# Kernel tuning notes

Hardware: AMD Instinct MI355X
Metric: run time of the kernel (lower is better)

The kernel has to match this reference:

```python
import jax, jax.numpy as jnp
import numpy as np

N_NODES = 10000
N_EDGES = 320000
D_FEAT = 128          # per-node feature dim -> in_dim = 2*D_FEAT = 256
OUT_DIM = 128
SCALES = 3


def setup_inputs() -> dict:
    key = jax.random.key(0)
    ks = jax.random.split(key, 7)
    node_features = jax.random.normal(ks[0], (N_NODES, D_FEAT), dtype=jnp.float32)
    temporal_info = jax.random.normal(ks[1], (N_NODES,), dtype=jnp.float32)
    in_dim_p1 = 2 * D_FEAT + 1  # 257: concat(src, dest) + temporal gap
    W1 = jax.random.normal(ks[2], (SCALES, in_dim_p1, OUT_DIM), dtype=jnp.float32) * 0.05
    b1 = jax.random.normal(ks[3], (SCALES, OUT_DIM), dtype=jnp.float32) * 0.05
    W2 = jax.random.normal(ks[4], (SCALES, OUT_DIM, OUT_DIM), dtype=jnp.float32) * 0.05
    b2 = jax.random.normal(ks[5], (SCALES, OUT_DIM), dtype=jnp.float32) * 0.05
    edge_index = jax.random.randint(ks[6], (2, N_EDGES), 0, N_NODES, dtype=jnp.int64)
    return {
        "node_features": node_features,
        "temporal_info": temporal_info,
        "W1": W1, "b1": b1, "W2": W2, "b2": b2,
        "edge_index": edge_index,
    }


def reference(node_features, temporal_info, W1, b1, W2, b2, edge_index):
    src, dest = edge_index[0], edge_index[1]
    # gather node pairs + temporal gap -> [E, 2*D+1]
    gap = (temporal_info[src] - temporal_info[dest])[:, None]
    edge_features = jnp.concatenate(
        [node_features[src], node_features[dest], gap], axis=-1)
    # all scales' 2-layer MLPs in one batched einsum; s = scale axis
    h = jax.nn.relu(jnp.einsum('ef,sfo->seo', edge_features, W1) + b1[:, None, :])
    tokens = jnp.einsum('seo,sop->sep', h, W2) + b2[:, None, :]  # [S, E, OUT]
    return tokens.mean(axis=0)  # mean over scales -> [E, OUT]
```

## Files before the change

### kernel.cpp

```cpp
#include <hip/hip_runtime.h>
#include <stdint.h>

#define NN 10000
#define NE 320000
#define DF 128
#define OD 128
#define NS 3

typedef __attribute__((ext_vector_type(8))) short bf16x8;
typedef __attribute__((ext_vector_type(16))) float f32x16;

static __device__ __forceinline__ uint32_t f2bf(float f) {
  uint32_t u = __float_as_uint(f);
  return (u + 0x7FFFu + ((u >> 16) & 1u)) >> 16;
}
static __device__ __forceinline__ float bflo(uint32_t u) { return __uint_as_float(u << 16); }
static __device__ __forceinline__ float bfhi(uint32_t u) { return __uint_as_float(u & 0xFFFF0000u); }

static __device__ __forceinline__ uint32_t relu2(uint32_t a, uint32_t d) {
  float f0 = fmaxf(bflo(a) + bflo(d), 0.0f);
  float f1 = fmaxf(bfhi(a) + bfhi(d), 0.0f);
  return f2bf(f0) | (f2bf(f1) << 16);
}

__global__ __launch_bounds__(256) void prep_w2(
    const float* __restrict__ W2, const float* __restrict__ b2,
    unsigned short* __restrict__ w2t, float* __restrict__ bmean)
{
  int tid = blockIdx.x * 256 + threadIdx.x;
  if (tid < NS * OD * OD) {
    int s = tid / (OD * OD);
    int r = tid % (OD * OD);
    int k = r / OD;
    int n = r % OD;
    w2t[(s * OD + n) * OD + k] = (unsigned short)f2bf(W2[tid]);
  }
  if (tid < OD) bmean[tid] = (b2[tid] + b2[OD + tid] + b2[2 * OD + tid]) * (1.0f / 3.0f);
}

__global__ __launch_bounds__(256) void node_proj(
    const float* __restrict__ nf, const float* __restrict__ temporal,
    const float* __restrict__ W1, const float* __restrict__ b1,
    unsigned short* __restrict__ Qsrc, unsigned short* __restrict__ Qdst)
{
  __shared__ unsigned short Asm[8 * 64 * 8];
  __shared__ unsigned short Bsm[4 * 8 * 64 * 8];
  __shared__ float tsh[32];

  const int t = threadIdx.x;
  const int m0 = blockIdx.x * 32;
  const int c = blockIdx.y;
  const int s = c >> 1, proj = c & 1;

  if (t < 32) {
    int node = m0 + t;
    tsh[t] = (node < NN) ? temporal[node] : 0.0f;
  }

  {
    int m = t >> 3, j16 = t & 7;
    int node = m0 + m;
    float v[16];
    if (node < NN) {
      const float4* p = (const float4*)(nf + (size_t)node * DF + j16 * 16);
      #pragma unroll
      for (int i = 0; i < 4; i++) {
        float4 x = p[i];
        v[4 * i] = x.x; v[4 * i + 1] = x.y; v[4 * i + 2] = x.z; v[4 * i + 3] = x.w;
      }
    } else {
      #pragma unroll
      for (int i = 0; i < 16; i++) v[i] = 0.0f;
    }
    uint32_t pk[8];
    #pragma unroll
    for (int i = 0; i < 8; i++) pk[i] = f2bf(v[2 * i]) | (f2bf(v[2 * i + 1]) << 16);
    uint32_t* d0 = (uint32_t*)(Asm + (j16 * 64 + m) * 8);
    uint32_t* d1 = (uint32_t*)(Asm + (j16 * 64 + 32 + m) * 8);
    d0[0] = pk[0]; d0[1] = pk[1]; d0[2] = pk[2]; d0[3] = pk[3];
    d1[0] = pk[4]; d1[1] = pk[5]; d1[2] = pk[6]; d1[3] = pk[7];
  }

  {
    int o = t & 127, qh = t >> 7;
    const float* wbase = W1 + (size_t)(s * 257 + proj * 128) * OD + o;
    int nt = o >> 5, lnlo = o & 31;
    #pragma unroll
    for (int r = 0; r < 8; r++) {
      int kh = qh * 8 + r;
      float v[8];
      #pragma unroll
      for (int j = 0; j < 8; j++) v[j] = wbase[(size_t)(kh * 8 + j) * OD];
      uint32_t pk[4];
      #pragma unroll
      for (int i = 0; i < 4; i++) pk[i] = f2bf(v[2 * i]) | (f2bf(v[2 * i + 1]) << 16);
      int q = kh >> 1, half = kh & 1;
      uint32_t* d = (uint32_t*)(Bsm + ((nt * 8 + q) * 64 + half * 32 + lnlo) * 8);
      d[0] = pk[0]; d[1] = pk[1]; d[2] = pk[2]; d[3] = pk[3];
    }
  }
  __syncthreads();

  const int lane = t & 63, w = t >> 6;
  f32x16 C;
  #pragma unroll
  for (int i = 0; i < 16; i++) C[i] = 0.0f;
  #pragma unroll
  for (int q = 0; q < 8; q++) {
    bf16x8 a = *(const bf16x8*)(Asm + (q * 64 + lane) * 8);
    bf16x8 b = *(const bf16x8*)(Bsm + ((w * 8 + q) * 64 + lane) * 8);
    C = __builtin_amdgcn_mfma_f32_32x32x16_bf16(a, b, C, 0, 0, 0);
  }

  const int o = w * 32 + (lane & 31);
  const float w1gv = W1[(size_t)(s * 257 + 256) * OD + o];
  const float b1v = b1[s * OD + o];
  unsigned short* Qt = (proj == 0) ? Qsrc : Qdst;
  #pragma unroll
  for (int r = 0; r < 16; r++) {
    int row = (r & 3) + 8 * (r >> 2) + 4 * (lane >> 5);
    int node = m0 + row;
    if (node < NN) {
      float val = C[r];
      if (proj == 0) val += b1v + tsh[row] * w1gv;
      else           val -= tsh[row] * w1gv;
      Qt[(size_t)node * (NS * OD) + s * OD + o] = (unsigned short)f2bf(val);
    }
  }
}

__global__ __launch_bounds__(256) void edge_mlp(
    const unsigned short* __restrict__ Qsrc, const unsigned short* __restrict__ Qdst,
    const unsigned short* __restrict__ W2T, const float* __restrict__ bmean,
    const int* __restrict__ ei, float* __restrict__ out)
{
  __shared__ unsigned short hsm[NS * 8 * 64 * 8];

  const int t = threadIdx.x;
  const int lane = t & 63, w = t >> 6;
  const int nlo = lane & 31, khi = lane >> 5;

  bf16x8 bfrag[NS][8];
  {
    int n = w * 32 + nlo;
    #pragma unroll
    for (int s = 0; s < NS; s++) {
      const unsigned short* base = W2T + ((s * OD + n) * OD + khi * 8);
      #pragma unroll
      for (int q = 0; q < 8; q++)
        bfrag[s][q] = *(const bf16x8*)(base + q * 16);
    }
  }
  const float bmv = bmean[w * 32 + nlo];

  const int m = t >> 3, j16 = t & 7;

  for (int tt = 0; tt < 4; tt++) {
    const int e0 = blockIdx.x * 128 + tt * 32;
    {
      const int e = e0 + m;
      const int srcn = ei[e];
      const int dstn = ei[NE + e];
      const unsigned short* ps = Qsrc + (size_t)srcn * (NS * OD) + j16 * 16;
      const unsigned short* pd = Qdst + (size_t)dstn * (NS * OD) + j16 * 16;
      #pragma unroll
      for (int s = 0; s < NS; s++) {
        uint4 a0 = *(const uint4*)(ps + s * OD);
        uint4 a1 = *(const uint4*)(ps + s * OD + 8);
        uint4 d0 = *(const uint4*)(pd + s * OD);
        uint4 d1 = *(const uint4*)(pd + s * OD + 8);
        uint4 w0, w1;
        w0.x = relu2(a0.x, d0.x); w0.y = relu2(a0.y, d0.y);
        w0.z = relu2(a0.z, d0.z); w0.w = relu2(a0.w, d0.w);
        w1.x = relu2(a1.x, d1.x); w1.y = relu2(a1.y, d1.y);
        w1.z = relu2(a1.z, d1.z); w1.w = relu2(a1.w, d1.w);
        *(uint4*)(hsm + ((s * 8 + j16) * 64 + m) * 8) = w0;
        *(uint4*)(hsm + ((s * 8 + j16) * 64 + 32 + m) * 8) = w1;
      }
    }
    __syncthreads();

    f32x16 C;
    #pragma unroll
    for (int i = 0; i < 16; i++) C[i] = 0.0f;
    #pragma unroll
    for (int s = 0; s < NS; s++) {
      #pragma unroll
      for (int q = 0; q < 8; q++) {
        bf16x8 a = *(const bf16x8*)(hsm + ((s * 8 + q) * 64 + lane) * 8);
        C = __builtin_amdgcn_mfma_f32_32x32x16_bf16(a, bfrag[s][q], C, 0, 0, 0);
      }
    }

    #pragma unroll
    for (int r = 0; r < 16; r++) {
      int row = (r & 3) + 8 * (r >> 2) + 4 * khi;
      out[(size_t)(e0 + row) * OD + w * 32 + nlo] = C[r] * (1.0f / 3.0f) + bmv;
    }
    __syncthreads();
  }
}

extern "C" void kernel_launch(void* const* d_in, const int* in_sizes, int n_in,
                              void* d_out, int out_size, void* d_ws, size_t ws_size,
                              hipStream_t stream) {
  const float* nf       = (const float*)d_in[0];
  const float* temporal = (const float*)d_in[1];
  const float* W1       = (const float*)d_in[2];
  const float* b1       = (const float*)d_in[3];
  const float* W2       = (const float*)d_in[4];
  const float* b2       = (const float*)d_in[5];
  const int*   ei       = (const int*)d_in[6];
  float* out = (float*)d_out;

  char* ws = (char*)d_ws;
  unsigned short* Qsrc = (unsigned short*)ws;
  unsigned short* Qdst = (unsigned short*)(ws + 7680000);
  unsigned short* W2T  = (unsigned short*)(ws + 15360000);
  float*          bmv  = (float*)(ws + 15360000 + 98304);

  prep_w2 <<<dim3(192),     dim3(256), 0, stream>>>(W2, b2, W2T, bmv);
  node_proj<<<dim3(313, 6), dim3(256), 0, stream>>>(nf, temporal, W1, b1, Qsrc, Qdst);
  edge_mlp <<<dim3(2500),   dim3(256), 0, stream>>>(Qsrc, Qdst, W2T, bmv, ei, out);
}
```

Before: 302.5 us.

## Prefetch edge gathers across tiles, swizzle LDS, amortize W1 staging in node_proj

In edge_mlp, all edge indices are loaded up front and the Q gathers for the next 32-edge tile are issued into registers before the MFMA phase of the current tile, so global gather latency overlaps with compute. LDS layouts for the hidden tile and the node-feature tile are XOR-swizzled by k-chunk to reduce bank conflicts. node_proj now loops over 8 node tiles per block with the converted W1 slice held in LDS, amortizing the W1 load and bf16 conversion. The cost is higher register pressure from the double-buffered gather registers, which may reduce occupancy, and fewer node_proj blocks.

```diff
diff --git a/kernel.cpp b/kernel.cpp
--- a/kernel.cpp
+++ b/kernel.cpp
@@ -48,38 +48,8 @@
   __shared__ float tsh[32];
 
   const int t = threadIdx.x;
-  const int m0 = blockIdx.x * 32;
   const int c = blockIdx.y;
   const int s = c >> 1, proj = c & 1;
-
-  if (t < 32) {
-    int node = m0 + t;
-    tsh[t] = (node < NN) ? temporal[node] : 0.0f;
-  }
-
-  {
-    int m = t >> 3, j16 = t & 7;
-    int node = m0 + m;
-    float v[16];
-    if (node < NN) {
-      const float4* p = (const float4*)(nf + (size_t)node * DF + j16 * 16);
-      #pragma unroll
-      for (int i = 0; i < 4; i++) {
-        float4 x = p[i];
-        v[4 * i] = x.x; v[4 * i + 1] = x.y; v[4 * i + 2] = x.z; v[4 * i + 3] = x.w;
-      }
-    } else {
-      #pragma unroll
-      for (int i = 0; i < 16; i++) v[i] = 0.0f;
-    }
-    uint32_t pk[8];
-    #pragma unroll
-    for (int i = 0; i < 8; i++) pk[i] = f2bf(v[2 * i]) | (f2bf(v[2 * i + 1]) << 16);
-    uint32_t* d0 = (uint32_t*)(Asm + (j16 * 64 + m) * 8);
-    uint32_t* d1 = (uint32_t*)(Asm + (j16 * 64 + 32 + m) * 8);
-    d0[0] = pk[0]; d0[1] = pk[1]; d0[2] = pk[2]; d0[3] = pk[3];
-    d1[0] = pk[4]; d1[1] = pk[5]; d1[2] = pk[6]; d1[3] = pk[7];
-  }
 
   {
     int o = t & 127, qh = t >> 7;
@@ -99,33 +69,66 @@
       d[0] = pk[0]; d[1] = pk[1]; d[2] = pk[2]; d[3] = pk[3];
     }
   }
-  __syncthreads();
 
   const int lane = t & 63, w = t >> 6;
-  f32x16 C;
-  #pragma unroll
-  for (int i = 0; i < 16; i++) C[i] = 0.0f;
-  #pragma unroll
-  for (int q = 0; q < 8; q++) {
-    bf16x8 a = *(const bf16x8*)(Asm + (q * 64 + lane) * 8);
-    bf16x8 b = *(const bf16x8*)(Bsm + ((w * 8 + q) * 64 + lane) * 8);
-    C = __builtin_amdgcn_mfma_f32_32x32x16_bf16(a, b, C, 0, 0, 0);
-  }
-
   const int o = w * 32 + (lane & 31);
   const float w1gv = W1[(size_t)(s * 257 + 256) * OD + o];
   const float b1v = b1[s * OD + o];
   unsigned short* Qt = (proj == 0) ? Qsrc : Qdst;
-  #pragma unroll
-  for (int r = 0; r < 16; r++) {
-    int row = (r & 3) + 8 * (r >> 2) + 4 * (lane >> 5);
-    int node = m0 + row;
-    if (node < NN) {
-      float val = C[r];
-      if (proj == 0) val += b1v + tsh[row] * w1gv;
-      else           val -= tsh[row] * w1gv;
-      Qt[(size_t)node * (NS * OD) + s * OD + o] = (unsigned short)f2bf(val);
-    }
+  const int m = t >> 3, j16 = t & 7;
+
+  for (int it = 0; it < 8; it++) {
+    const int m0 = (blockIdx.x * 8 + it) * 32;
+    if (m0 >= NN) break;
+
+    if (t < 32) tsh[t] = (m0 + t < NN) ? temporal[m0 + t] : 0.0f;
+
+    {
+      int node = m0 + m;
+      float v[16];
+      if (node < NN) {
+        const float4* p = (const float4*)(nf + (size_t)node * DF + j16 * 16);
+        #pragma unroll
+        for (int i = 0; i < 4; i++) {
+          float4 x = p[i];
+          v[4 * i] = x.x; v[4 * i + 1] = x.y; v[4 * i + 2] = x.z; v[4 * i + 3] = x.w;
+        }
+      } else {
+        #pragma unroll
+        for (int i = 0; i < 16; i++) v[i] = 0.0f;
+      }
+      uint32_t pk[8];
+      #pragma unroll
+      for (int i = 0; i < 8; i++) pk[i] = f2bf(v[2 * i]) | (f2bf(v[2 * i + 1]) << 16);
+      uint32_t* d0 = (uint32_t*)(Asm + (j16 * 64 + (m ^ j16)) * 8);
+      uint32_t* d1 = (uint32_t*)(Asm + (j16 * 64 + ((32 + m) ^ j16)) * 8);
+      d0[0] = pk[0]; d0[1] = pk[1]; d0[2] = pk[2]; d0[3] = pk[3];
+      d1[0] = pk[4]; d1[1] = pk[5]; d1[2] = pk[6]; d1[3] = pk[7];
+    }
+    __syncthreads();
+
+    f32x16 C;
+    #pragma unroll
+    for (int i = 0; i < 16; i++) C[i] = 0.0f;
+    #pragma unroll
+    for (int q = 0; q < 8; q++) {
+      bf16x8 a = *(const bf16x8*)(Asm + (q * 64 + (lane ^ q)) * 8);
+      bf16x8 b = *(const bf16x8*)(Bsm + ((w * 8 + q) * 64 + lane) * 8);
+      C = __builtin_amdgcn_mfma_f32_32x32x16_bf16(a, b, C, 0, 0, 0);
+    }
+
+    #pragma unroll
+    for (int r = 0; r < 16; r++) {
+      int row = (r & 3) + 8 * (r >> 2) + 4 * (lane >> 5);
+      int node = m0 + row;
+      if (node < NN) {
+        float val = C[r];
+        if (proj == 0) val += b1v + tsh[row] * w1gv;
+        else           val -= tsh[row] * w1gv;
+        Qt[(size_t)node * (NS * OD) + s * OD + o] = (unsigned short)f2bf(val);
+      }
+    }
+    __syncthreads();
   }
 }
 
@@ -155,27 +158,53 @@
 
   const int m = t >> 3, j16 = t & 7;
 
+  int sn[4], dn[4];
+  #pragma unroll
+  for (int tt = 0; tt < 4; tt++) {
+    int e = blockIdx.x * 128 + tt * 32 + m;
+    sn[tt] = ei[e];
+    dn[tt] = ei[NE + e];
+  }
+
+  uint4 G[12], G2[12];
+  {
+    const unsigned short* ps = Qsrc + (size_t)sn[0] * (NS * OD) + j16 * 16;
+    const unsigned short* pd = Qdst + (size_t)dn[0] * (NS * OD) + j16 * 16;
+    #pragma unroll
+    for (int s = 0; s < NS; s++) {
+      G[4 * s + 0] = *(const uint4*)(ps + s * OD);
+      G[4 * s + 1] = *(const uint4*)(ps + s * OD + 8);
+      G[4 * s + 2] = *(const uint4*)(pd + s * OD);
+      G[4 * s + 3] = *(const uint4*)(pd + s * OD + 8);
+    }
+  }
+
+  #pragma unroll
   for (int tt = 0; tt < 4; tt++) {
     const int e0 = blockIdx.x * 128 + tt * 32;
-    {
-      const int e = e0 + m;
-      const int srcn = ei[e];
-      const int dstn = ei[NE + e];
-      const unsigned short* ps = Qsrc + (size_t)srcn * (NS * OD) + j16 * 16;
-      const unsigned short* pd = Qdst + (size_t)dstn * (NS * OD) + j16 * 16;
+
+    #pragma unroll
+    for (int s = 0; s < NS; s++) {
+      uint4 a0 = G[4 * s + 0], a1 = G[4 * s + 1];
+      uint4 d0 = G[4 * s + 2], d1 = G[4 * s + 3];
+      uint4 w0, w1;
+      w0.x = relu2(a0.x, d0.x); w0.y = relu2(a0.y, d0.y);
+      w0.z = relu2(a0.z, d0.z); w0.w = relu2(a0.w, d0.w);
+      w1.x = relu2(a1.x, d1.x); w1.y = relu2(a1.y, d1.y);
+      w1.z = relu2(a1.z, d1.z); w1.w = relu2(a1.w, d1.w);
+      *(uint4*)(hsm + ((s * 8 + j16) * 64 + (m ^ j16)) * 8) = w0;
+      *(uint4*)(hsm + ((s * 8 + j16) * 64 + ((32 + m) ^ j16)) * 8) = w1;
+    }
+
+    if (tt < 3) {
+      const unsigned short* ps = Qsrc + (size_t)sn[tt + 1] * (NS * OD) + j16 * 16;
+      const unsigned short* pd = Qdst + (size_t)dn[tt + 1] * (NS * OD) + j16 * 16;
       #pragma unroll
       for (int s = 0; s < NS; s++) {
-        uint4 a0 = *(const uint4*)(ps + s * OD);
-        uint4 a1 = *(const uint4*)(ps + s * OD + 8);
-        uint4 d0 = *(const uint4*)(pd + s * OD);
-        uint4 d1 = *(const uint4*)(pd + s * OD + 8);
-        uint4 w0, w1;
-        w0.x = relu2(a0.x, d0.x); w0.y = relu2(a0.y, d0.y);
-        w0.z = relu2(a0.z, d0.z); w0.w = relu2(a0.w, d0.w);
-        w1.x = relu2(a1.x, d1.x); w1.y = relu2(a1.y, d1.y);
-        w1.z = relu2(a1.z, d1.z); w1.w = relu2(a1.w, d1.w);
-        *(uint4*)(hsm + ((s * 8 + j16) * 64 + m) * 8) = w0;
-        *(uint4*)(hsm + ((s * 8 + j16) * 64 + 32 + m) * 8) = w1;
+        G2[4 * s + 0] = *(const uint4*)(ps + s * OD);
+        G2[4 * s + 1] = *(const uint4*)(ps + s * OD + 8);
+        G2[4 * s + 2] = *(const uint4*)(pd + s * OD);
+        G2[4 * s + 3] = *(const uint4*)(pd + s * OD + 8);
       }
     }
     __syncthreads();
@@ -187,7 +216,7 @@
     for (int s = 0; s < NS; s++) {
       #pragma unroll
       for (int q = 0; q < 8; q++) {
-        bf16x8 a = *(const bf16x8*)(hsm + ((s * 8 + q) * 64 + lane) * 8);
+        bf16x8 a = *(const bf16x8*)(hsm + ((s * 8 + q) * 64 + (lane ^ q)) * 8);
         C = __builtin_amdgcn_mfma_f32_32x32x16_bf16(a, bfrag[s][q], C, 0, 0, 0);
       }
     }
@@ -198,6 +227,9 @@
       out[(size_t)(e0 + row) * OD + w * 32 + nlo] = C[r] * (1.0f / 3.0f) + bmv;
     }
     __syncthreads();
+
+    #pragma unroll
+    for (int i = 0; i < 12; i++) G[i] = G2[i];
   }
 }
 
@@ -219,7 +251,7 @@
   unsigned short* W2T  = (unsigned short*)(ws + 15360000);
   float*          bmv  = (float*)(ws + 15360000 + 98304);
 
-  prep_w2 <<<dim3(192),     dim3(256), 0, stream>>>(W2, b2, W2T, bmv);
-  node_proj<<<dim3(313, 6), dim3(256), 0, stream>>>(nf, temporal, W1, b1, Qsrc, Qdst);
-  edge_mlp <<<dim3(2500),   dim3(256), 0, stream>>>(Qsrc, Qdst, W2T, bmv, ei, out);
-}
+  prep_w2 <<<dim3(192),    dim3(256), 0, stream>>>(W2, b2, W2T, bmv);
+  node_proj<<<dim3(40, 6), dim3(256), 0, stream>>>(nf, temporal, W1, b1, Qsrc, Qdst);
+  edge_mlp <<<dim3(2500),  dim3(256), 0, stream>>>(Qsrc, Qdst, W2T, bmv, ei, out);
+}
```

New measurement: 266.8 us. 11.8% less time.
